# Optimization experiments

Hardware: AMD Instinct MI355X
Metric: run time of the kernel (lower is better)

Reference implementation:

```python
import jax, jax.numpy as jnp
import numpy as np

N = 100000      # n_nodes
D = 64          # in_features == out_features (elementwise W mul requires equality)
DEG = 16        # avg degree for random edges
H = 2           # n_head
ALPHA = 0.2     # LeakyReLU negative slope


def setup_inputs() -> dict:
    key = jax.random.key(0)
    k1, k2, k3 = jax.random.split(key, 3)
    inputs = jax.random.normal(k1, (N, D), dtype=jnp.float32)
    # random edges + self-loops so every row has at least one edge (nonzero rowsum)
    rnd = jax.random.randint(k2, (2, N * DEG), 0, N)
    self_loops = jnp.tile(jnp.arange(N)[None, :], (2, 1))
    edge_index = jnp.concatenate([self_loops, rnd], axis=1)  # [2, 1.7M]
    # per-head params, matching torch init: W = ones, a ~ U(-stdv, stdv)
    W = jnp.ones((H, D), dtype=jnp.float32)
    stdv = 1.0 / np.sqrt(D * 2)
    a = jax.random.uniform(k3, (H, 2 * D), dtype=jnp.float32, minval=-stdv, maxval=stdv)
    return {"inputs": inputs, "edge_index": edge_index, "W": W, "a": a}


def reference(inputs, edge_index, W, a):
    n = inputs.shape[0]
    row, col = edge_index[0], edge_index[1]

    def head(Wh, ah):
        h = inputs * Wh  # [N, D]
        # a @ [h_src; h_dst] decomposes into per-node dots, then scalar edge gather
        score = (h @ ah[:D])[row] + (h @ ah[D:])[col]          # [E]
        e = jnp.exp(jnp.where(score > 0, score, ALPHA * score))  # exp(leaky_relu)
        rowsum = jax.ops.segment_sum(e, row, num_segments=n)     # [N]
        # sparse.mm(coo(edge, e), inputs): h_prime[i] = sum_j e_ij * inputs[j]
        h_prime = jax.ops.segment_sum(e[:, None] * inputs[col], row, num_segments=n)
        return h_prime / rowsum[:, None]

    outs = jax.vmap(head)(W, a)  # [H, N, D]
    return outs.mean(axis=0)
```

## Files before the change

### kernel.cpp

```cpp
#include <hip/hip_runtime.h>


#define D 64
#define ALPHA 0.2f
#define CAP 96
#define BSHIFT 9
#define BROWS 512
#define MAXBUK 256
#define TILE 2048
#define PACKSHIFT 23
#define COLMASK ((1u << PACKSHIFT) - 1u)

__device__ __forceinline__ unsigned bf16rne(float f) {
    unsigned u = __float_as_uint(f);
    u += 0x7fffu + ((u >> 16) & 1u);
    return u >> 16;
}

__global__ __launch_bounds__(256) void k_node_scores(
    const float* __restrict__ x, const float* __restrict__ W,
    const float* __restrict__ a, float4* __restrict__ s, int N)
{
    int wid  = (blockIdx.x * blockDim.x + threadIdx.x) >> 6;
    int lane = threadIdx.x & 63;
    if (wid >= N) return;
    float v  = x[(size_t)wid * D + lane];
    float h0 = v * W[lane];
    float h1 = v * W[D + lane];
    float t0 = h0 * a[lane];
    float t1 = h0 * a[D + lane];
    float t2 = h1 * a[2 * D + lane];
    float t3 = h1 * a[3 * D + lane];
#pragma unroll
    for (int off = 32; off; off >>= 1) {
        t0 += __shfl_xor(t0, off);
        t1 += __shfl_xor(t1, off);
        t2 += __shfl_xor(t2, off);
        t3 += __shfl_xor(t3, off);
    }
    if (lane == 0) s[wid] = make_float4(t0, t1, t2, t3);
}

__global__ __launch_bounds__(256) void k_tobf16(
    const float2* __restrict__ x, unsigned* __restrict__ xh2, int M)
{
    int i = blockIdx.x * 256 + threadIdx.x;
    if (i >= M) return;
    float2 f = x[i];
    xh2[i] = (bf16rne(f.y) << 16) | bf16rne(f.x);
}

__global__ __launch_bounds__(256) void k_bucket_hist(
    const int* __restrict__ row, int* __restrict__ bcnt, int E, int nbuk)
{
    __shared__ int h[MAXBUK];
    for (int i = threadIdx.x; i < nbuk; i += 256) h[i] = 0;
    __syncthreads();
    int stride = gridDim.x * 256;
    for (int i = blockIdx.x * 256 + threadIdx.x; i < E; i += stride)
        atomicAdd(&h[row[i] >> BSHIFT], 1);
    __syncthreads();
    for (int i = threadIdx.x; i < nbuk; i += 256)
        if (h[i]) atomicAdd(&bcnt[i], h[i]);
}

__global__ void k_bucket_scan(const int* __restrict__ bcnt,
                              int* __restrict__ bbase, int* __restrict__ bcur, int nbuk)
{
    __shared__ int sd[MAXBUK];
    int t = threadIdx.x;
    int v = (t < nbuk) ? bcnt[t] : 0;
    sd[t] = v;
    __syncthreads();
    for (int off = 1; off < MAXBUK; off <<= 1) {
        int add = (t >= off) ? sd[t - off] : 0;
        __syncthreads();
        sd[t] += add;
        __syncthreads();
    }
    if (t < nbuk) { bbase[t] = sd[t] - v; bcur[t] = sd[t] - v; }
    if (t == nbuk - 1) bbase[nbuk] = sd[t];
}

__global__ __launch_bounds__(256) void k_binning(
    const int* __restrict__ row, const int* __restrict__ col,
    int* __restrict__ bcur, unsigned* __restrict__ ebuf, int E, int nbuk)
{
    __shared__ int lrow[TILE];
    __shared__ int lcol[TILE];
    __shared__ int h[MAXBUK];
    __shared__ int st[MAXBUK];
    __shared__ int gb[MAXBUK];
    __shared__ int cur[MAXBUK];
    __shared__ int sd[MAXBUK];
    int t = threadIdx.x;
    int base = blockIdx.x * TILE;
    int cnt_tile = E - base; if (cnt_tile > TILE) cnt_tile = TILE;

    for (int i = t; i < nbuk; i += 256) h[i] = 0;
    __syncthreads();

    int r[8], c[8], b[8];
#pragma unroll
    for (int j = 0; j < 8; j++) {
        int li = j * 256 + t;
        if (li < cnt_tile) {
            int idx = base + li;
            r[j] = row[idx]; c[j] = col[idx]; b[j] = r[j] >> BSHIFT;
            atomicAdd(&h[b[j]], 1);
        } else b[j] = -1;
    }
    __syncthreads();

    if (t < MAXBUK) sd[t] = (t < nbuk) ? h[t] : 0;
    __syncthreads();
    for (int off = 1; off < MAXBUK; off <<= 1) {
        int add = (t < MAXBUK && t >= off) ? sd[t - off] : 0;
        __syncthreads();
        if (t < MAXBUK) sd[t] += add;
        __syncthreads();
    }
    if (t < nbuk) {
        int start = sd[t] - h[t];
        st[t]  = start;
        cur[t] = start;
        gb[t]  = h[t] ? atomicAdd(&bcur[t], h[t]) : 0;
    }
    __syncthreads();

#pragma unroll
    for (int j = 0; j < 8; j++) {
        if (b[j] >= 0) {
            int p = atomicAdd(&cur[b[j]], 1);
            lrow[p] = r[j]; lcol[p] = c[j];
        }
    }
    __syncthreads();

    for (int i = t; i < cnt_tile; i += 256) {
        int rr = lrow[i];
        int bb = rr >> BSHIFT;
        int g  = gb[bb] + (i - st[bb]);
        ebuf[g] = ((unsigned)(rr & (BROWS - 1)) << PACKSHIFT) | (unsigned)lcol[i];
    }
}

__global__ __launch_bounds__(256) void k_rowsort(
    const unsigned* __restrict__ ebuf, const int* __restrict__ bbase,
    int* __restrict__ offsets, int* __restrict__ counts,
    int* __restrict__ scol, int N)
{
    __shared__ int hist[BROWS];
    __shared__ int offs[BROWS];
    __shared__ int wsum[256];
    int b = blockIdx.x, t = threadIdx.x;
    int lo = b << BSHIFT;
    int s0 = bbase[b], s1 = bbase[b + 1];

    for (int j = t; j < BROWS; j += 256) hist[j] = 0;
    __syncthreads();
    for (int i = s0 + t; i < s1; i += 256)
        atomicAdd(&hist[ebuf[i] >> PACKSHIFT], 1);
    __syncthreads();

    int a0 = hist[2 * t], a1 = hist[2 * t + 1];
    int s = a0 + a1;
    wsum[t] = s;
    __syncthreads();
    for (int off = 1; off < 256; off <<= 1) {
        int add = (t >= off) ? wsum[t - off] : 0;
        __syncthreads();
        wsum[t] += add;
        __syncthreads();
    }
    int run = wsum[t] - s;
    offs[2 * t]     = run;
    offs[2 * t + 1] = run + a0;
    __syncthreads();

    for (int j = t; j < BROWS; j += 256) {
        int rg = lo + j;
        if (rg < N) { offsets[rg] = s0 + offs[j]; counts[rg] = hist[j]; }
    }
    __syncthreads();
    for (int j = t; j < BROWS; j += 256) hist[j] = offs[j];
    __syncthreads();

    for (int i = s0 + t; i < s1; i += 256) {
        unsigned pk = ebuf[i];
        int p = atomicAdd(&hist[pk >> PACKSHIFT], 1);
        scol[s0 + p] = (int)(pk & COLMASK);
    }
}

__global__ __launch_bounds__(256) void k_gather(
    const unsigned* __restrict__ xh2, const float4* __restrict__ s,
    const int* __restrict__ offsets, const int* __restrict__ counts,
    const int* __restrict__ scol, float* __restrict__ out, int N)
{
    __shared__ int   lcol[4][CAP];
    __shared__ float le0[4][CAP];
    __shared__ float le1[4][CAP];
    int w    = threadIdx.x >> 6;
    int lane = threadIdx.x & 63;
    int n    = blockIdx.x * 4 + w;
    bool valid = (n < N);
    int start = 0, cnt = 0;
    float4 srow = make_float4(0.f, 0.f, 0.f, 0.f);
    if (valid) { start = offsets[n]; cnt = counts[n]; srow = s[n]; }

    float sum0 = 0.f, sum1 = 0.f;
    for (int k = lane; k < cnt; k += 64) {
        int c = scol[start + k];
        float4 sc = s[c];
        float sc0 = srow.x + sc.y;
        float sc1 = srow.z + sc.w;
        float e0 = __expf(sc0 > 0.f ? sc0 : ALPHA * sc0);
        float e1 = __expf(sc1 > 0.f ? sc1 : ALPHA * sc1);
        sum0 += e0; sum1 += e1;
        if (k < CAP) { lcol[w][k] = c; le0[w][k] = e0; le1[w][k] = e1; }
    }
    int m  = cnt < CAP ? cnt : CAP;
    int mp = (m + 7) & ~7;
    {
        int k = m + lane;
        if (k < mp) { lcol[w][k] = 0; le0[w][k] = 0.f; le1[w][k] = 0.f; }
    }
#pragma unroll
    for (int off = 32; off; off >>= 1) {
        sum0 += __shfl_xor(sum0, off);
        sum1 += __shfl_xor(sum1, off);
    }
    __syncthreads();
    if (!valid) return;
    float inv0 = 0.5f / sum0, inv1 = 0.5f / sum1;

    int half = lane >> 5;
    int li   = lane & 31;
    float acc0 = 0.f, acc1 = 0.f;
    for (int k = 0; k < mp; k += 8) {
#pragma unroll
        for (int j = 0; j < 4; j++) {
            int kk = k + 2 * j + half;
            int c = lcol[w][kk];
            float coef = inv0 * le0[w][kk] + inv1 * le1[w][kk];
            unsigned u = xh2[(size_t)c * 32 + li];
            acc0 += coef * __uint_as_float(u << 16);
            acc1 += coef * __uint_as_float(u & 0xffff0000u);
        }
    }
    for (int kk = CAP + half; kk < cnt; kk += 2) {
        int c = scol[start + kk];
        float4 sc = s[c];
        float sc0 = srow.x + sc.y, sc1 = srow.z + sc.w;
        float coef = inv0 * __expf(sc0 > 0.f ? sc0 : ALPHA * sc0)
                   + inv1 * __expf(sc1 > 0.f ? sc1 : ALPHA * sc1);
        unsigned u = xh2[(size_t)c * 32 + li];
        acc0 += coef * __uint_as_float(u << 16);
        acc1 += coef * __uint_as_float(u & 0xffff0000u);
    }
    acc0 += __shfl_xor(acc0, 32);
    acc1 += __shfl_xor(acc1, 32);
    if (half == 0) {
        float2* o = (float2*)(out + (size_t)n * D);
        o[li] = make_float2(acc0, acc1);
    }
}

extern "C" void kernel_launch(void* const* d_in, const int* in_sizes, int n_in,
                              void* d_out, int out_size, void* d_ws, size_t ws_size,
                              hipStream_t stream)
{
    const float* x  = (const float*)d_in[0];
    const int*   ei = (const int*)d_in[1];
    const float* W  = (const float*)d_in[2];
    const float* a  = (const float*)d_in[3];
    float*       out = (float*)d_out;
    int N = in_sizes[0] / D;
    int E = in_sizes[1] / 2;
    const int* row = ei;
    const int* col = ei + E;

    char* w = (char*)d_ws;
    float4*   s       = (float4*)w;   w += (size_t)N * sizeof(float4);
    int*      offsets = (int*)w;      w += (size_t)N * sizeof(int);
    int*      counts  = (int*)w;      w += (size_t)N * sizeof(int);
    int*      scol    = (int*)w;      w += (size_t)E * sizeof(int);
    unsigned* ebuf    = (unsigned*)w; w += (size_t)E * sizeof(unsigned);
    unsigned* xh2     = (unsigned*)w; w += (size_t)N * (D / 2) * sizeof(unsigned);
    int*      bcnt    = (int*)w;      w += MAXBUK * sizeof(int);
    int*      bbase   = (int*)w;      w += (MAXBUK + 4) * sizeof(int);
    int*      bcur    = (int*)w;      w += MAXBUK * sizeof(int);

    int NBUK = (N + BROWS - 1) >> BSHIFT;
    int M    = N * (D / 2);

    hipMemsetAsync(bcnt, 0, MAXBUK * sizeof(int), stream);
    k_node_scores<<<(N + 3) / 4, 256, 0, stream>>>(x, W, a, s, N);
    k_tobf16<<<(M + 255) / 256, 256, 0, stream>>>((const float2*)x, xh2, M);
    k_bucket_hist<<<256, 256, 0, stream>>>(row, bcnt, E, NBUK);
    k_bucket_scan<<<1, MAXBUK, 0, stream>>>(bcnt, bbase, bcur, NBUK);
    k_binning<<<(E + TILE - 1) / TILE, 256, 0, stream>>>(row, col, bcur, ebuf, E, NBUK);
    k_rowsort<<<NBUK, 256, 0, stream>>>(ebuf, bbase, offsets, counts, scol, N);
    k_gather<<<(N + 3) / 4, 256, 0, stream>>>(xh2, s, offsets, counts, scol, out, N);
}
```

Measured before the change: 226.7 us.

## Fuse bf16 cast into score kernel and replace atomic binning with tile scan

The bf16 conversion of node features moves into the per-node score kernel, removing a separate pass over x. Bucket offsets now come from per-tile histograms and a per-bucket column scan instead of global atomics, which removes the memset and makes the binning placement deterministic at the cost of one more kernel and a tile-count buffer. The row-sort kernel runs with 1024 threads per block. The gather kernel precomputes combined edge coefficients into a paired shared array so the inner loop does one shared load per edge, and drops a block barrier.

```diff
diff --git a/kernel.cpp b/kernel.cpp
--- a/kernel.cpp
+++ b/kernel.cpp
@@ -17,14 +17,16 @@
     return u >> 16;
 }
 
-__global__ __launch_bounds__(256) void k_node_scores(
+__global__ __launch_bounds__(256) void k_scores_cast(
     const float* __restrict__ x, const float* __restrict__ W,
-    const float* __restrict__ a, float4* __restrict__ s, int N)
+    const float* __restrict__ a, float4* __restrict__ s,
+    unsigned short* __restrict__ xh, int N)
 {
     int wid  = (blockIdx.x * blockDim.x + threadIdx.x) >> 6;
     int lane = threadIdx.x & 63;
     if (wid >= N) return;
-    float v  = x[(size_t)wid * D + lane];
+    float v = x[(size_t)wid * D + lane];
+    xh[(size_t)wid * D + lane] = (unsigned short)bf16rne(v);
     float h0 = v * W[lane];
     float h1 = v * W[D + lane];
     float t0 = h0 * a[lane];
@@ -41,31 +43,50 @@
     if (lane == 0) s[wid] = make_float4(t0, t1, t2, t3);
 }
 
-__global__ __launch_bounds__(256) void k_tobf16(
-    const float2* __restrict__ x, unsigned* __restrict__ xh2, int M)
-{
-    int i = blockIdx.x * 256 + threadIdx.x;
-    if (i >= M) return;
-    float2 f = x[i];
-    xh2[i] = (bf16rne(f.y) << 16) | bf16rne(f.x);
-}
-
-__global__ __launch_bounds__(256) void k_bucket_hist(
-    const int* __restrict__ row, int* __restrict__ bcnt, int E, int nbuk)
+__global__ __launch_bounds__(256) void k_tile_hist(
+    const int* __restrict__ row, unsigned short* __restrict__ tcnt, int E, int nbuk)
 {
     __shared__ int h[MAXBUK];
-    for (int i = threadIdx.x; i < nbuk; i += 256) h[i] = 0;
-    __syncthreads();
-    int stride = gridDim.x * 256;
-    for (int i = blockIdx.x * 256 + threadIdx.x; i < E; i += stride)
-        atomicAdd(&h[row[i] >> BSHIFT], 1);
-    __syncthreads();
-    for (int i = threadIdx.x; i < nbuk; i += 256)
-        if (h[i]) atomicAdd(&bcnt[i], h[i]);
+    int t = threadIdx.x, base = blockIdx.x * TILE;
+    int cnt = E - base; if (cnt > TILE) cnt = TILE;
+    for (int i = t; i < nbuk; i += 256) h[i] = 0;
+    __syncthreads();
+    for (int i = t; i < cnt; i += 256) atomicAdd(&h[row[base + i] >> BSHIFT], 1);
+    __syncthreads();
+    for (int i = t; i < nbuk; i += 256)
+        tcnt[(size_t)blockIdx.x * MAXBUK + i] = (unsigned short)h[i];
+}
+
+__global__ __launch_bounds__(256) void k_col_scan(
+    const unsigned short* __restrict__ tcnt, int* __restrict__ tbase,
+    int* __restrict__ bcnt, int NT, int nbuk)
+{
+    __shared__ int wsum[256];
+    int b = blockIdx.x, t = threadIdx.x;
+    int t4 = t * 4;
+    int v0 = (t4     < NT) ? tcnt[(size_t)(t4    ) * MAXBUK + b] : 0;
+    int v1 = (t4 + 1 < NT) ? tcnt[(size_t)(t4 + 1) * MAXBUK + b] : 0;
+    int v2 = (t4 + 2 < NT) ? tcnt[(size_t)(t4 + 2) * MAXBUK + b] : 0;
+    int v3 = (t4 + 3 < NT) ? tcnt[(size_t)(t4 + 3) * MAXBUK + b] : 0;
+    int sv = v0 + v1 + v2 + v3;
+    wsum[t] = sv;
+    __syncthreads();
+    for (int off = 1; off < 256; off <<= 1) {
+        int add = (t >= off) ? wsum[t - off] : 0;
+        __syncthreads();
+        wsum[t] += add;
+        __syncthreads();
+    }
+    int run = wsum[t] - sv;
+    if (t4     < NT) { tbase[(t4    ) * MAXBUK + b] = run; run += v0; }
+    if (t4 + 1 < NT) { tbase[(t4 + 1) * MAXBUK + b] = run; run += v1; }
+    if (t4 + 2 < NT) { tbase[(t4 + 2) * MAXBUK + b] = run; run += v2; }
+    if (t4 + 3 < NT) { tbase[(t4 + 3) * MAXBUK + b] = run; run += v3; }
+    if (t == 255) bcnt[b] = wsum[255];
 }
 
 __global__ void k_bucket_scan(const int* __restrict__ bcnt,
-                              int* __restrict__ bbase, int* __restrict__ bcur, int nbuk)
+                              int* __restrict__ bbase, int nbuk)
 {
     __shared__ int sd[MAXBUK];
     int t = threadIdx.x;
@@ -78,13 +99,14 @@
         sd[t] += add;
         __syncthreads();
     }
-    if (t < nbuk) { bbase[t] = sd[t] - v; bcur[t] = sd[t] - v; }
+    if (t < nbuk) bbase[t] = sd[t] - v;
     if (t == nbuk - 1) bbase[nbuk] = sd[t];
 }
 
 __global__ __launch_bounds__(256) void k_binning(
     const int* __restrict__ row, const int* __restrict__ col,
-    int* __restrict__ bcur, unsigned* __restrict__ ebuf, int E, int nbuk)
+    const int* __restrict__ bbase, const int* __restrict__ tbase,
+    unsigned* __restrict__ ebuf, int E, int nbuk)
 {
     __shared__ int lrow[TILE];
     __shared__ int lcol[TILE];
@@ -95,7 +117,7 @@
     __shared__ int sd[MAXBUK];
     int t = threadIdx.x;
     int base = blockIdx.x * TILE;
-    int cnt_tile = E - base; if (cnt_tile > TILE) cnt_tile = TILE;
+    int cnt = E - base; if (cnt > TILE) cnt = TILE;
 
     for (int i = t; i < nbuk; i += 256) h[i] = 0;
     __syncthreads();
@@ -104,7 +126,7 @@
 #pragma unroll
     for (int j = 0; j < 8; j++) {
         int li = j * 256 + t;
-        if (li < cnt_tile) {
+        if (li < cnt) {
             int idx = base + li;
             r[j] = row[idx]; c[j] = col[idx]; b[j] = r[j] >> BSHIFT;
             atomicAdd(&h[b[j]], 1);
@@ -112,19 +134,19 @@
     }
     __syncthreads();
 
-    if (t < MAXBUK) sd[t] = (t < nbuk) ? h[t] : 0;
+    sd[t] = (t < nbuk) ? h[t] : 0;
     __syncthreads();
     for (int off = 1; off < MAXBUK; off <<= 1) {
-        int add = (t < MAXBUK && t >= off) ? sd[t - off] : 0;
-        __syncthreads();
-        if (t < MAXBUK) sd[t] += add;
+        int add = (t >= off) ? sd[t - off] : 0;
+        __syncthreads();
+        sd[t] += add;
         __syncthreads();
     }
     if (t < nbuk) {
         int start = sd[t] - h[t];
         st[t]  = start;
         cur[t] = start;
-        gb[t]  = h[t] ? atomicAdd(&bcur[t], h[t]) : 0;
+        gb[t]  = bbase[t] + tbase[blockIdx.x * MAXBUK + t];
     }
     __syncthreads();
 
@@ -137,15 +159,15 @@
     }
     __syncthreads();
 
-    for (int i = t; i < cnt_tile; i += 256) {
+    for (int i = t; i < cnt; i += 256) {
         int rr = lrow[i];
         int bb = rr >> BSHIFT;
-        int g  = gb[bb] + (i - st[bb]);
-        ebuf[g] = ((unsigned)(rr & (BROWS - 1)) << PACKSHIFT) | (unsigned)lcol[i];
-    }
-}
-
-__global__ __launch_bounds__(256) void k_rowsort(
+        ebuf[gb[bb] + (i - st[bb])] =
+            ((unsigned)(rr & (BROWS - 1)) << PACKSHIFT) | (unsigned)lcol[i];
+    }
+}
+
+__global__ __launch_bounds__(1024) void k_rowsort(
     const unsigned* __restrict__ ebuf, const int* __restrict__ bbase,
     int* __restrict__ offsets, int* __restrict__ counts,
     int* __restrict__ scol, int N)
@@ -157,36 +179,34 @@
     int lo = b << BSHIFT;
     int s0 = bbase[b], s1 = bbase[b + 1];
 
-    for (int j = t; j < BROWS; j += 256) hist[j] = 0;
-    __syncthreads();
-    for (int i = s0 + t; i < s1; i += 256)
+    if (t < BROWS) hist[t] = 0;
+    __syncthreads();
+    for (int i = s0 + t; i < s1; i += 1024)
         atomicAdd(&hist[ebuf[i] >> PACKSHIFT], 1);
     __syncthreads();
 
-    int a0 = hist[2 * t], a1 = hist[2 * t + 1];
-    int s = a0 + a1;
-    wsum[t] = s;
+    int a0 = 0, a1 = 0, sv = 0;
+    if (t < 256) { a0 = hist[2 * t]; a1 = hist[2 * t + 1]; sv = a0 + a1; wsum[t] = sv; }
     __syncthreads();
     for (int off = 1; off < 256; off <<= 1) {
-        int add = (t >= off) ? wsum[t - off] : 0;
-        __syncthreads();
-        wsum[t] += add;
-        __syncthreads();
-    }
-    int run = wsum[t] - s;
-    offs[2 * t]     = run;
-    offs[2 * t + 1] = run + a0;
-    __syncthreads();
-
-    for (int j = t; j < BROWS; j += 256) {
-        int rg = lo + j;
-        if (rg < N) { offsets[rg] = s0 + offs[j]; counts[rg] = hist[j]; }
-    }
-    __syncthreads();
-    for (int j = t; j < BROWS; j += 256) hist[j] = offs[j];
-    __syncthreads();
-
-    for (int i = s0 + t; i < s1; i += 256) {
+        int add = 0;
+        if (t < 256 && t >= off) add = wsum[t - off];
+        __syncthreads();
+        if (t < 256) wsum[t] += add;
+        __syncthreads();
+    }
+    if (t < 256) { int run = wsum[t] - sv; offs[2 * t] = run; offs[2 * t + 1] = run + a0; }
+    __syncthreads();
+
+    if (t < BROWS) {
+        int rg = lo + t;
+        if (rg < N) { offsets[rg] = s0 + offs[t]; counts[rg] = hist[t]; }
+    }
+    __syncthreads();
+    if (t < BROWS) hist[t] = offs[t];
+    __syncthreads();
+
+    for (int i = s0 + t; i < s1; i += 1024) {
         unsigned pk = ebuf[i];
         int p = atomicAdd(&hist[pk >> PACKSHIFT], 1);
         scol[s0 + p] = (int)(pk & COLMASK);
@@ -198,9 +218,9 @@
     const int* __restrict__ offsets, const int* __restrict__ counts,
     const int* __restrict__ scol, float* __restrict__ out, int N)
 {
-    __shared__ int   lcol[4][CAP];
-    __shared__ float le0[4][CAP];
-    __shared__ float le1[4][CAP];
+    __shared__ float  le0[4][CAP];
+    __shared__ float  le1[4][CAP];
+    __shared__ float2 lpair[4][CAP];
     int w    = threadIdx.x >> 6;
     int lane = threadIdx.x & 63;
     int n    = blockIdx.x * 4 + w;
@@ -218,22 +238,23 @@
         float e0 = __expf(sc0 > 0.f ? sc0 : ALPHA * sc0);
         float e1 = __expf(sc1 > 0.f ? sc1 : ALPHA * sc1);
         sum0 += e0; sum1 += e1;
-        if (k < CAP) { lcol[w][k] = c; le0[w][k] = e0; le1[w][k] = e1; }
+        if (k < CAP) { lpair[w][k].x = __int_as_float(c); le0[w][k] = e0; le1[w][k] = e1; }
     }
     int m  = cnt < CAP ? cnt : CAP;
     int mp = (m + 7) & ~7;
     {
         int k = m + lane;
-        if (k < mp) { lcol[w][k] = 0; le0[w][k] = 0.f; le1[w][k] = 0.f; }
+        if (k < mp) { lpair[w][k].x = __int_as_float(0); le0[w][k] = 0.f; le1[w][k] = 0.f; }
     }
 #pragma unroll
     for (int off = 32; off; off >>= 1) {
         sum0 += __shfl_xor(sum0, off);
         sum1 += __shfl_xor(sum1, off);
     }
-    __syncthreads();
     if (!valid) return;
     float inv0 = 0.5f / sum0, inv1 = 0.5f / sum1;
+    for (int k = lane; k < mp; k += 64)
+        lpair[w][k].y = inv0 * le0[w][k] + inv1 * le1[w][k];
 
     int half = lane >> 5;
     int li   = lane & 31;
@@ -242,11 +263,11 @@
 #pragma unroll
         for (int j = 0; j < 4; j++) {
             int kk = k + 2 * j + half;
-            int c = lcol[w][kk];
-            float coef = inv0 * le0[w][kk] + inv1 * le1[w][kk];
-            unsigned u = xh2[(size_t)c * 32 + li];
-            acc0 += coef * __uint_as_float(u << 16);
-            acc1 += coef * __uint_as_float(u & 0xffff0000u);
+            float2 pr = lpair[w][kk];
+            int c = __float_as_int(pr.x);
+            unsigned u = xh2[((unsigned)c << 5) + li];
+            acc0 += pr.y * __uint_as_float(u << 16);
+            acc1 += pr.y * __uint_as_float(u & 0xffff0000u);
         }
     }
     for (int kk = CAP + half; kk < cnt; kk += 2) {
@@ -255,7 +276,7 @@
         float sc0 = srow.x + sc.y, sc1 = srow.z + sc.w;
         float coef = inv0 * __expf(sc0 > 0.f ? sc0 : ALPHA * sc0)
                    + inv1 * __expf(sc1 > 0.f ? sc1 : ALPHA * sc1);
-        unsigned u = xh2[(size_t)c * 32 + li];
+        unsigned u = xh2[((unsigned)c << 5) + li];
         acc0 += coef * __uint_as_float(u << 16);
         acc1 += coef * __uint_as_float(u & 0xffff0000u);
     }
@@ -281,26 +302,26 @@
     const int* row = ei;
     const int* col = ei + E;
 
+    int NBUK = (N + BROWS - 1) >> BSHIFT;
+    int NT   = (E + TILE - 1) / TILE;
+
     char* w = (char*)d_ws;
-    float4*   s       = (float4*)w;   w += (size_t)N * sizeof(float4);
-    int*      offsets = (int*)w;      w += (size_t)N * sizeof(int);
-    int*      counts  = (int*)w;      w += (size_t)N * sizeof(int);
-    int*      scol    = (int*)w;      w += (size_t)E * sizeof(int);
-    unsigned* ebuf    = (unsigned*)w; w += (size_t)E * sizeof(unsigned);
-    unsigned* xh2     = (unsigned*)w; w += (size_t)N * (D / 2) * sizeof(unsigned);
-    int*      bcnt    = (int*)w;      w += MAXBUK * sizeof(int);
-    int*      bbase   = (int*)w;      w += (MAXBUK + 4) * sizeof(int);
-    int*      bcur    = (int*)w;      w += MAXBUK * sizeof(int);
-
-    int NBUK = (N + BROWS - 1) >> BSHIFT;
-    int M    = N * (D / 2);
-
-    hipMemsetAsync(bcnt, 0, MAXBUK * sizeof(int), stream);
-    k_node_scores<<<(N + 3) / 4, 256, 0, stream>>>(x, W, a, s, N);
-    k_tobf16<<<(M + 255) / 256, 256, 0, stream>>>((const float2*)x, xh2, M);
-    k_bucket_hist<<<256, 256, 0, stream>>>(row, bcnt, E, NBUK);
-    k_bucket_scan<<<1, MAXBUK, 0, stream>>>(bcnt, bbase, bcur, NBUK);
-    k_binning<<<(E + TILE - 1) / TILE, 256, 0, stream>>>(row, col, bcur, ebuf, E, NBUK);
-    k_rowsort<<<NBUK, 256, 0, stream>>>(ebuf, bbase, offsets, counts, scol, N);
-    k_gather<<<(N + 3) / 4, 256, 0, stream>>>(xh2, s, offsets, counts, scol, out, N);
-}
+    float4*         s       = (float4*)w;         w += (size_t)N * sizeof(float4);
+    int*            offsets = (int*)w;            w += (size_t)N * sizeof(int);
+    int*            counts  = (int*)w;            w += (size_t)N * sizeof(int);
+    int*            scol    = (int*)w;            w += (size_t)E * sizeof(int);
+    unsigned*       ebuf    = (unsigned*)w;       w += (size_t)E * sizeof(unsigned);
+    int*            tbase   = (int*)w;            w += (size_t)NT * MAXBUK * sizeof(int);
+    int*            bcnt    = (int*)w;            w += MAXBUK * sizeof(int);
+    int*            bbase   = (int*)w;            w += (MAXBUK + 4) * sizeof(int);
+    unsigned short* xh      = (unsigned short*)w; w += (size_t)N * D * sizeof(unsigned short);
+    unsigned short* tcnt    = (unsigned short*)w; w += (size_t)NT * MAXBUK * sizeof(unsigned short);
+
+    k_scores_cast<<<(N + 3) / 4, 256, 0, stream>>>(x, W, a, s, xh, N);
+    k_tile_hist<<<NT, 256, 0, stream>>>(row, tcnt, E, NBUK);
+    k_col_scan<<<NBUK, 256, 0, stream>>>(tcnt, tbase, bcnt, NT, NBUK);
+    k_bucket_scan<<<1, MAXBUK, 0, stream>>>(bcnt, bbase, NBUK);
+    k_binning<<<NT, 256, 0, stream>>>(row, col, bbase, tbase, ebuf, E, NBUK);
+    k_rowsort<<<NBUK, 1024, 0, stream>>>(ebuf, bbase, offsets, counts, scol, N);
+    k_gather<<<(N + 3) / 4, 256, 0, stream>>>((const unsigned*)xh, s, offsets, counts, scol, out, N);
+}
```

New measurement: 208.6 us. 8.0% less time.
